# Optimization experiments

Hardware: AMD Instinct MI355X
Metric: run time of the kernel (lower is better)

Reference implementation:

```python
import jax, jax.numpy as jnp
import numpy as np

D_MODEL = 1024
N_HEADS = 8
D_HEAD = 64
D_FF = 4096
LAMBDA_INIT = 0.8
EPS = 1e-5


def _ln(x, g, b):
    m = jnp.mean(x, axis=-1, keepdims=True)
    v = jnp.mean(jnp.square(x - m), axis=-1, keepdims=True)
    return (x - m) * jax.lax.rsqrt(v + EPS) * g + b


def setup_inputs() -> dict:
    key = jax.random.key(0)
    ks = jax.random.split(key, 24)
    D, H, Dh, F = D_MODEL, N_HEADS, D_HEAD, D_FF
    P = 2 * H * Dh  # projection width for q/k/v (== D here)
    s = lambda fan: 1.0 / np.sqrt(fan)
    inp = {
        'x': jax.random.normal(ks[0], (2, 2048, D), jnp.float32),
        'ln1_g': jnp.ones((D,), jnp.float32), 'ln1_b': jnp.zeros((D,), jnp.float32),
        'ln2_g': jnp.ones((D,), jnp.float32), 'ln2_b': jnp.zeros((D,), jnp.float32),
        'Wq': jax.random.normal(ks[1], (D, P), jnp.float32) * s(D), 'bq': jnp.zeros((P,), jnp.float32),
        'Wk': jax.random.normal(ks[2], (D, P), jnp.float32) * s(D), 'bk': jnp.zeros((P,), jnp.float32),
        'Wv': jax.random.normal(ks[3], (D, P), jnp.float32) * s(D), 'bv': jnp.zeros((P,), jnp.float32),
        'Wo': jax.random.normal(ks[4], (P, D), jnp.float32) * s(P), 'bo': jnp.zeros((D,), jnp.float32),
        'lq1': jax.random.normal(ks[5], (H, Dh), jnp.float32) * 0.1,
        'lk1': jax.random.normal(ks[6], (H, Dh), jnp.float32) * 0.1,
        'lq2': jax.random.normal(ks[7], (H, Dh), jnp.float32) * 0.1,
        'lk2': jax.random.normal(ks[8], (H, Dh), jnp.float32) * 0.1,
        'gn_w': jnp.ones((P,), jnp.float32), 'gn_b': jnp.zeros((P,), jnp.float32),
        'W1': jax.random.normal(ks[9], (D, F), jnp.float32) * s(D), 'b1': jnp.zeros((F,), jnp.float32),
        'Wg': jax.random.normal(ks[10], (F, F), jnp.float32) * s(F), 'bg': jnp.zeros((F,), jnp.float32),
        'W2': jax.random.normal(ks[11], (F, D), jnp.float32) * s(F), 'b2': jnp.zeros((D,), jnp.float32),
    }
    return inp


def reference(x, ln1_g, ln1_b, ln2_g, ln2_b, Wq, bq, Wk, bk, Wv, bv, Wo, bo,
              lq1, lk1, lq2, lk2, gn_w, gn_b, W1, b1, Wg, bg, W2, b2):
    B, S, D = x.shape
    H, Dh = N_HEADS, D_HEAD
    scale = 1.0 / np.sqrt(Dh)

    # --- differential attention sublayer (pre-norm) ---
    h = _ln(x, ln1_g, ln1_b)
    q = (h @ Wq + bq).reshape(B, S, H, 2, Dh)
    k = (h @ Wk + bk).reshape(B, S, H, 2, Dh)
    v = (h @ Wv + bv).reshape(B, S, H, 2 * Dh)

    A1 = jax.nn.softmax(jnp.einsum('bshd,bthd->bhst', q[..., 0, :], k[..., 0, :]) * scale, axis=-1)
    A2 = jax.nn.softmax(jnp.einsum('bshd,bthd->bhst', q[..., 1, :], k[..., 1, :]) * scale, axis=-1)

    lam = (jnp.exp(jnp.sum(lq1 * lk1, axis=-1))
           - jnp.exp(jnp.sum(lq2 * lk2, axis=-1)) + LAMBDA_INIT)  # [H]
    diff = A1 - lam[None, :, None, None] * A2                     # [B,H,S,S]
    o = jnp.einsum('bhst,bthe->bshe', diff, v)                    # [B,S,H,2*Dh]

    # headwise GroupNorm over the 2*Dh channels of each head
    mu = jnp.mean(o, axis=-1, keepdims=True)
    var = jnp.mean(jnp.square(o - mu), axis=-1, keepdims=True)
    o = (o - mu) * jax.lax.rsqrt(var + EPS)
    o = o * gn_w.reshape(H, 2 * Dh) + gn_b.reshape(H, 2 * Dh)
    o = o * (1.0 - LAMBDA_INIT)

    attn_out = o.reshape(B, S, 2 * H * Dh) @ Wo + bo
    x = x + attn_out

    # --- FFN sublayer: note source applies prenorm2 BEFORE residual split ---
    x = _ln(x, ln2_g, ln2_b)
    u = x @ W1 + b1
    u = u * jax.nn.silu(u @ Wg + bg)   # swiGLU gate
    return x + (u @ W2 + b2)
```

## Files before the change

### kernel.cpp

```cpp
#include <hip/hip_runtime.h>
#include <hip/hip_bf16.h>


typedef __attribute__((ext_vector_type(8))) __bf16 bf16x8;
typedef __attribute__((ext_vector_type(4))) float f32x4;

#define GAS __attribute__((address_space(1)))
#define LAS __attribute__((address_space(3)))

__device__ __forceinline__ unsigned short f2bf(float f) {
  unsigned u = __float_as_uint(f);
  u += 0x7fffu + ((u >> 16) & 1u);
  return (unsigned short)(u >> 16);
}
__device__ __forceinline__ float bf2f(unsigned short s) {
  return __uint_as_float(((unsigned)s) << 16);
}

__global__ __launch_bounds__(256)
void transpose_cvt(const float* __restrict__ W, unsigned short* __restrict__ WT,
                   int K, int N, float scale) {
  __shared__ float tile[64][65];
  const int n0 = blockIdx.x * 64, k0 = blockIdx.y * 64;
  const int tr = threadIdx.x >> 4, tc = (threadIdx.x & 15) * 4;
#pragma unroll
  for (int i = 0; i < 4; ++i) {
    const float4 v = *(const float4*)&W[(size_t)(k0 + tr + i * 16) * N + n0 + tc];
    tile[tr + i * 16][tc + 0] = v.x;
    tile[tr + i * 16][tc + 1] = v.y;
    tile[tr + i * 16][tc + 2] = v.z;
    tile[tr + i * 16][tc + 3] = v.w;
  }
  __syncthreads();
#pragma unroll
  for (int i = 0; i < 4; ++i) {
    const int n = tr + i * 16;
    ushort4 o;
    o.x = f2bf(tile[tc + 0][n] * scale);
    o.y = f2bf(tile[tc + 1][n] * scale);
    o.z = f2bf(tile[tc + 2][n] * scale);
    o.w = f2bf(tile[tc + 3][n] * scale);
    *(ushort4*)&WT[(size_t)(n0 + n) * K + k0 + tc] = o;
  }
}

__global__ void prep_bias(const float* __restrict__ bq, const float* __restrict__ bk,
                          const float* __restrict__ bv, float* __restrict__ out,
                          float qscale) {
  const int i = blockIdx.x * 256 + threadIdx.x;
  if (i < 1024) out[i] = bq[i] * qscale;
  else if (i < 2048) out[i] = bk[i - 1024];
  else out[i] = bv[i - 2048];
}

__global__ __launch_bounds__(256)
void v_transpose(const unsigned short* __restrict__ v, unsigned short* __restrict__ VT) {
  __shared__ unsigned short tile[64][65];
  const int s0 = blockIdx.x * 64, e0 = blockIdx.y * 64, bh = blockIdx.z;
  const int b = bh >> 3, h = bh & 7;
  const int tr = threadIdx.x >> 4, tc = (threadIdx.x & 15) * 4;
  const size_t inbase = (size_t)b * 2048 * 3072 + h * 128;
#pragma unroll
  for (int i = 0; i < 4; ++i) {
    const int r = tr + i * 16;
    const ushort4 val = *(const ushort4*)&v[inbase + (size_t)(s0 + r) * 3072 + e0 + tc];
    tile[r][tc + 0] = val.x;
    tile[r][tc + 1] = val.y;
    tile[r][tc + 2] = val.z;
    tile[r][tc + 3] = val.w;
  }
  __syncthreads();
#pragma unroll
  for (int i = 0; i < 4; ++i) {
    const int n = tr + i * 16;
    ushort4 oo;
    oo.x = tile[tc + 0][n];
    oo.y = tile[tc + 1][n];
    oo.z = tile[tc + 2][n];
    oo.w = tile[tc + 3][n];
    *(ushort4*)&VT[(size_t)(bh * 128 + e0 + n) * 2048 + s0 + tc] = oo;
  }
}

__global__ void lam_kernel(const float* __restrict__ lq1, const float* __restrict__ lk1,
                           const float* __restrict__ lq2, const float* __restrict__ lk2,
                           float* __restrict__ lam) {
  const int w = threadIdx.x >> 6, d = threadIdx.x & 63;
  float a = lq1[w * 64 + d] * lk1[w * 64 + d];
  float c = lq2[w * 64 + d] * lk2[w * 64 + d];
#pragma unroll
  for (int off = 32; off; off >>= 1) {
    a += __shfl_xor(a, off);
    c += __shfl_xor(c, off);
  }
  if (d == 0) lam[w] = __expf(a) - __expf(c) + 0.8f;
}

template <int WRITE_F32>
__global__ __launch_bounds__(256)
void ln_kernel(const float* __restrict__ x, const float* __restrict__ g,
               const float* __restrict__ bsh, unsigned short* __restrict__ obf,
               float* __restrict__ of32) {
  __shared__ float red[16];
  const int row = blockIdx.x, tid = threadIdx.x;
  const float4 v = *(const float4*)&x[(size_t)row * 1024 + tid * 4];
  float s = v.x + v.y + v.z + v.w;
  float q = v.x * v.x + v.y * v.y + v.z * v.z + v.w * v.w;
#pragma unroll
  for (int off = 32; off; off >>= 1) {
    s += __shfl_xor(s, off);
    q += __shfl_xor(q, off);
  }
  if ((tid & 63) == 0) {
    red[tid >> 6] = s;
    red[8 + (tid >> 6)] = q;
  }
  __syncthreads();
  s = red[0] + red[1] + red[2] + red[3];
  q = red[8] + red[9] + red[10] + red[11];
  const float mean = s * (1.f / 1024.f);
  const float var = q * (1.f / 1024.f) - mean * mean;
  const float rstd = rsqrtf(var + 1e-5f);
  const float4 gg = *(const float4*)&g[tid * 4];
  const float4 bb = *(const float4*)&bsh[tid * 4];
  float y0 = (v.x - mean) * rstd * gg.x + bb.x;
  float y1 = (v.y - mean) * rstd * gg.y + bb.y;
  float y2 = (v.z - mean) * rstd * gg.z + bb.z;
  float y3 = (v.w - mean) * rstd * gg.w + bb.w;
  const size_t base = (size_t)row * 1024 + tid * 4;
  ushort4 o;
  o.x = f2bf(y0); o.y = f2bf(y1); o.z = f2bf(y2); o.w = f2bf(y3);
  *(ushort4*)&obf[base] = o;
  if (WRITE_F32) {
    *(float4*)&of32[base] = make_float4(y0, y1, y2, y3);
  }
}

template <int EPI>
__global__ __launch_bounds__(256)
void gemm_bf16(const unsigned short* __restrict__ A,
               const unsigned short* __restrict__ BT,
               const float* __restrict__ bias,
               const float* __restrict__ res,
               const unsigned short* __restrict__ gate_u,
               void* __restrict__ Cout, int M, int N, int K, float bscale) {
  __shared__ unsigned short ldsA[2][128 * 32];
  __shared__ unsigned short ldsB[2][128 * 32];
  const int tid = threadIdx.x;
  const int wv = tid >> 6, ln = tid & 63, lg = ln >> 4, lc = ln & 15;
  const int wm = wv >> 1, wn = wv & 1;
  const int nwg = gridDim.x * gridDim.y;
  const int linear = blockIdx.y * gridDim.x + blockIdx.x;
  const int swz = (linear & 7) * (nwg >> 3) + (linear >> 3);
  const int m0 = (swz / gridDim.x) * 128, n0 = (swz % gridDim.x) * 128;
  const int rsub = ln >> 2, acol = (ln & 3) * 8;

  f32x4 acc[4][4];
#pragma unroll
  for (int i = 0; i < 4; ++i)
#pragma unroll
    for (int j = 0; j < 4; ++j) acc[i][j] = (f32x4)0.f;

  auto stage = [&](int buf, int k0) {
#pragma unroll
    for (int j = 0; j < 2; ++j) {
      const int rowblk = wv * 32 + j * 16;
      const unsigned short* ga = A + (size_t)(m0 + rowblk + rsub) * K + (k0 + acol);
      __builtin_amdgcn_global_load_lds((GAS void*)ga,
          (LAS void*)&ldsA[buf][rowblk * 32], 16, 0, 0);
      const unsigned short* gb = BT + (size_t)(n0 + rowblk + rsub) * K + (k0 + acol);
      __builtin_amdgcn_global_load_lds((GAS void*)gb,
          (LAS void*)&ldsB[buf][rowblk * 32], 16, 0, 0);
    }
  };

  const int nk = K / 32;
  stage(0, 0);
  int cur = 0;
  for (int i = 0; i < nk; ++i) {
    if (i + 1 < nk) {
      stage(cur ^ 1, (i + 1) * 32);
      asm volatile("s_waitcnt vmcnt(4)" ::: "memory");
    } else {
      asm volatile("s_waitcnt vmcnt(0)" ::: "memory");
    }
    __builtin_amdgcn_s_barrier();
    bf16x8 af[4], bf[4];
#pragma unroll
    for (int m = 0; m < 4; ++m)
      af[m] = *(const bf16x8*)&ldsA[cur][(wm * 64 + m * 16 + lc) * 32 + lg * 8];
#pragma unroll
    for (int n = 0; n < 4; ++n)
      bf[n] = *(const bf16x8*)&ldsB[cur][(wn * 64 + n * 16 + lc) * 32 + lg * 8];
    __builtin_amdgcn_s_setprio(1);
#pragma unroll
    for (int m = 0; m < 4; ++m)
#pragma unroll
      for (int n = 0; n < 4; ++n)
        acc[m][n] = __builtin_amdgcn_mfma_f32_16x16x32_bf16(af[m], bf[n], acc[m][n], 0, 0, 0);
    __builtin_amdgcn_s_setprio(0);
    __builtin_amdgcn_s_barrier();
    cur ^= 1;
  }

#pragma unroll
  for (int m = 0; m < 4; ++m) {
#pragma unroll
    for (int n = 0; n < 4; ++n) {
      const int c = n0 + wn * 64 + n * 16 + lc;
      const float bc = bias[c] * bscale;
#pragma unroll
      for (int j = 0; j < 4; ++j) {
        const int r = m0 + wm * 64 + m * 16 + lg * 4 + j;
        const size_t idx = (size_t)r * N + c;
        const float v = acc[m][n][j] + bc;
        if (EPI == 0) {
          ((unsigned short*)Cout)[idx] = f2bf(v);
        } else if (EPI == 1) {
          ((float*)Cout)[idx] = res[idx] + v;
        } else {
          const float uu = bf2f(gate_u[idx]);
          const float sw = v / (1.f + __expf(-v));
          ((unsigned short*)Cout)[idx] = f2bf(uu * sw);
        }
      }
    }
  }
}

template <int EPI>
__global__ __launch_bounds__(512)
void gemm256(const unsigned short* __restrict__ A,
             const unsigned short* __restrict__ BT,
             const float* __restrict__ bias,
             const unsigned short* __restrict__ gate_u,
             unsigned short* __restrict__ Cout, int M, int N, int K) {
  __shared__ unsigned short lds[65536];
  const int tid = threadIdx.x;
  const int w = tid >> 6, ln = tid & 63, lg = ln >> 4, lc = ln & 15;
  const int wm = w >> 2, wn = w & 3;
  const int nwg = gridDim.x * gridDim.y;
  const int linear = blockIdx.y * gridDim.x + blockIdx.x;
  const int swzb = (linear & 7) * (nwg >> 3) + (linear >> 3);
  const int m0 = (swzb / gridDim.x) * 256, n0 = (swzb % gridDim.x) * 256;

  f32x4 acc[8][4];
#pragma unroll
  for (int i = 0; i < 8; ++i)
#pragma unroll
    for (int j = 0; j < 4; ++j) acc[i][j] = (f32x4)0.f;

  auto stage_half = [&](int tensor, int j, int hh) {
    const unsigned short* base = tensor ? BT : A;
    const int row0 = (tensor ? n0 : m0) + hh * 128;
    const int slot = tensor * 4 + (j & 1) * 2 + hh;
#pragma unroll
    for (int c = 0; c < 2; ++c) {
      const int chunk = w * 2 + c;
      const int L = chunk * 1024 + ln * 16;
      const int r = L >> 7, inner = L & 127;
      const char* src = (const char*)(base + (size_t)(row0 + r) * K + j * 64) +
                        (inner ^ ((r & 7) << 4));
      __builtin_amdgcn_global_load_lds((GAS void*)src,
          (LAS void*)((char*)lds + slot * 16384 + chunk * 1024), 16, 0, 0);
    }
  };
  auto read_a = [&](int j, int mf, int ks) -> bf16x8 {
    const int r = mf * 16 + lc;
    const int slot = (j & 1) * 2 + wm;
    const int cb = ks * 64 + lg * 16;
    return *(const bf16x8*)((const char*)lds + slot * 16384 + r * 128 +
                            (cb ^ ((r & 7) << 4)));
  };
  auto read_b = [&](int j, int nf, int ks) -> bf16x8 {
    const int R = wn * 64 + nf * 16 + lc;
    const int slot = 4 + (j & 1) * 2 + (R >> 7);
    const int r = R & 127;
    const int cb = ks * 64 + lg * 16;
    return *(const bf16x8*)((const char*)lds + slot * 16384 + r * 128 +
                            (cb ^ ((r & 7) << 4)));
  };

  const int nkt = K / 64;

  stage_half(0, 0, 0); stage_half(0, 0, 1);
  stage_half(1, 0, 0); stage_half(1, 0, 1);
  stage_half(1, 1, 0); stage_half(1, 1, 1);
  asm volatile("s_waitcnt vmcnt(0)" ::: "memory");
  __builtin_amdgcn_s_barrier();

  bf16x8 bfr[4][2];
  for (int it = 0; it < nkt / 2; ++it) {
    const int J = it * 2;
#pragma unroll
    for (int half = 0; half < 2; ++half) {
      const int jc = J + half;
#pragma unroll
      for (int q = 0; q < 4; ++q) {
        if (q == 0) {
#pragma unroll
          for (int nf = 0; nf < 4; ++nf)
#pragma unroll
            for (int ks = 0; ks < 2; ++ks) bfr[nf][ks] = read_b(jc, nf, ks);
        }
        bf16x8 afr[2][2];
#pragma unroll
        for (int mm = 0; mm < 2; ++mm)
#pragma unroll
          for (int ks = 0; ks < 2; ++ks) afr[mm][ks] = read_a(jc, q * 2 + mm, ks);
        if (half == 0) {
          if (q == 0) stage_half(0, J + 1, 0);
          if (q == 1) stage_half(0, J + 1, 1);
          if (q == 2 && J + 2 < nkt) stage_half(1, J + 2, 0);
          if (q == 3 && J + 2 < nkt) stage_half(1, J + 2, 1);
        } else {
          if (q == 0 && J + 2 < nkt) stage_half(0, J + 2, 0);
          if (q == 1 && J + 2 < nkt) stage_half(0, J + 2, 1);
          if (q == 2 && J + 3 < nkt) stage_half(1, J + 3, 0);
          if (q == 3 && J + 3 < nkt) stage_half(1, J + 3, 1);
        }
        if (q == 0) asm volatile("s_waitcnt lgkmcnt(8)" ::: "memory");
        if (q == 3) asm volatile("s_waitcnt vmcnt(4)" ::: "memory");
        __builtin_amdgcn_s_barrier();
        __builtin_amdgcn_s_setprio(1);
#pragma unroll
        for (int mm = 0; mm < 2; ++mm)
#pragma unroll
          for (int nf = 0; nf < 4; ++nf)
#pragma unroll
            for (int ks = 0; ks < 2; ++ks)
              acc[q * 2 + mm][nf] = __builtin_amdgcn_mfma_f32_16x16x32_bf16(
                  afr[mm][ks], bfr[nf][ks], acc[q * 2 + mm][nf], 0, 0, 0);
        __builtin_amdgcn_s_setprio(0);
        __builtin_amdgcn_s_barrier();
      }
    }
  }

#pragma unroll
  for (int mf = 0; mf < 8; ++mf) {
#pragma unroll
    for (int nf = 0; nf < 4; ++nf) {
      const int c = n0 + wn * 64 + nf * 16 + lc;
      const float bc = bias[c];
#pragma unroll
      for (int jj = 0; jj < 4; ++jj) {
        const int r = m0 + wm * 128 + mf * 16 + lg * 4 + jj;
        const size_t idx = (size_t)r * N + c;
        const float v = acc[mf][nf][jj] + bc;
        if (EPI == 0) {
          Cout[idx] = f2bf(v);
        } else {
          const float uu = bf2f(gate_u[idx]);
          const float sw = v / (1.f + __expf(-v));
          Cout[idx] = f2bf(uu * sw);
        }
      }
    }
  }
}

__global__ __launch_bounds__(256)
void attn_kernel(const unsigned short* __restrict__ q,
                 const unsigned short* __restrict__ k,
                 const unsigned short* __restrict__ VT,
                 float* __restrict__ Opart,
                 float* __restrict__ lsumPart) {
  constexpr int S = 2048;
  constexpr int QS = 3072;
  __shared__ unsigned short k_tile[2][32 * 128];
  __shared__ unsigned short v_tile[2][128 * 32];
  __shared__ unsigned short p_lds[4][2][512];
  const int tid = threadIdx.x, w = tid >> 6, ln = tid & 63, lg = ln >> 4, lc = ln & 15;
  const int id = blockIdx.x;
  const int bh = (id & 7) + 8 * ((id >> 9) & 1);
  const int qt = (id >> 3) & 31;
  const int tcn = (id >> 8) & 1;
  const size_t chan = (size_t)(bh >> 3) * S * QS + (bh & 7) * 128;
  const size_t vtbase = (size_t)bh * 128 * S;
  const int qrow = qt * 64 + w * 16 + lc;

  bf16x8 qf[2][2];
#pragma unroll
  for (int p = 0; p < 2; ++p)
#pragma unroll
    for (int ks = 0; ks < 2; ++ks)
      qf[p][ks] = *(const bf16x8*)&q[chan + (size_t)qrow * QS + p * 64 + ks * 32 + lg * 8];

  f32x4 O[2][8];
#pragma unroll
  for (int p = 0; p < 2; ++p)
#pragma unroll
    for (int ef = 0; ef < 8; ++ef) O[p][ef] = (f32x4)0.f;
  float lsum[2][4];
#pragma unroll
  for (int p = 0; p < 2; ++p)
#pragma unroll
    for (int j = 0; j < 4; ++j) lsum[p][j] = 0.f;

  const int prd = ((lc * 64 + lg * 16) ^ ((lc & 7) << 4)) >> 1;

  auto stage = [&](int buf, int t0) {
#pragma unroll
    for (int c = 0; c < 2; ++c) {
      {
        const int L = (w * 2 + c) * 1024 + ln * 16;
        const int r = L >> 8, inner = L & 255;
        const char* src = (const char*)(k + chan + (size_t)(t0 + r) * QS) +
                          (inner ^ ((r & 7) << 4));
        __builtin_amdgcn_global_load_lds((GAS void*)src,
            (LAS void*)((char*)&k_tile[buf][0] + (w * 2 + c) * 1024), 16, 0, 0);
      }
      {
        const int L = (w * 2 + c) * 1024 + ln * 16;
        const int e = L >> 6, inner = L & 63;
        const char* src = (const char*)(VT + vtbase + (size_t)e * S + t0) +
                          (inner ^ ((e & 3) << 4));
        __builtin_amdgcn_global_load_lds((GAS void*)src,
            (LAS void*)((char*)&v_tile[buf][0] + (w * 2 + c) * 1024), 16, 0, 0);
      }
    }
  };

  auto compute = [&](int buf) {
    const char* kb = (const char*)&k_tile[buf][0];
    const char* vb = (const char*)&v_tile[buf][0];
    bf16x8 vf[8];
#pragma unroll
    for (int ef = 0; ef < 8; ++ef) {
      const int e = ef * 16 + lc;
      vf[ef] = *(const bf16x8*)(vb + e * 64 + ((lg * 16) ^ ((e & 3) << 4)));
    }
#pragma unroll
    for (int p = 0; p < 2; ++p) {
      bf16x8 kf[2][2];
#pragma unroll
      for (int tf = 0; tf < 2; ++tf) {
        const int r = tf * 16 + lc;
#pragma unroll
        for (int ks = 0; ks < 2; ++ks)
          kf[tf][ks] = *(const bf16x8*)(kb + r * 256 +
                          ((p * 128 + ks * 64 + lg * 16) ^ ((r & 7) << 4)));
      }
      f32x4 sfr[2];
      __builtin_amdgcn_s_setprio(1);
#pragma unroll
      for (int tf = 0; tf < 2; ++tf) {
        f32x4 acc = (f32x4)0.f;
#pragma unroll
        for (int ks = 0; ks < 2; ++ks)
          acc = __builtin_amdgcn_mfma_f32_16x16x32_bf16(qf[p][ks], kf[tf][ks], acc, 0, 0, 0);
        sfr[tf] = acc;
      }
      __builtin_amdgcn_s_setprio(0);

#pragma unroll
      for (int tf = 0; tf < 2; ++tf)
#pragma unroll
        for (int j = 0; j < 4; ++j) {
          const float e = __expf(sfr[tf][j]);
          lsum[p][j] += e;
          const int qq = lg * 4 + j;
          const int wi = ((qq * 64 + (tf * 16 + lc) * 2) ^ ((qq & 7) << 4)) >> 1;
          p_lds[w][p][wi] = f2bf(e);
        }

      const bf16x8 pa = *(const bf16x8*)&p_lds[w][p][prd];
      __builtin_amdgcn_s_setprio(1);
#pragma unroll
      for (int ef = 0; ef < 8; ++ef)
        O[p][ef] = __builtin_amdgcn_mfma_f32_16x16x32_bf16(pa, vf[ef], O[p][ef], 0, 0, 0);
      __builtin_amdgcn_s_setprio(0);
    }
  };

  const int tbeg = tcn * (S / 2);
  stage(0, tbeg);
  int cur = 0;
  for (int it = 0; it < 32; ++it) {
    if (it < 31) {
      stage(cur ^ 1, tbeg + (it + 1) * 32);
      asm volatile("s_waitcnt vmcnt(4)" ::: "memory");
    } else {
      asm volatile("s_waitcnt vmcnt(0)" ::: "memory");
    }
    __builtin_amdgcn_s_barrier();
    compute(cur);
    __builtin_amdgcn_s_barrier();
    cur ^= 1;
  }

  const size_t rowbase = ((size_t)tcn * 16 + bh) * S;
#pragma unroll
  for (int p = 0; p < 2; ++p)
#pragma unroll
    for (int j = 0; j < 4; ++j) {
      float s = lsum[p][j];
      s += __shfl_xor(s, 1);
      s += __shfl_xor(s, 2);
      s += __shfl_xor(s, 4);
      s += __shfl_xor(s, 8);
      const int row = qt * 64 + w * 16 + lg * 4 + j;
      if (lc == 0)
        lsumPart[(rowbase + row) * 2 + p] = s;
#pragma unroll
      for (int ef = 0; ef < 8; ++ef)
        Opart[(rowbase + row) * 256 + p * 128 + ef * 16 + lc] = O[p][ef][j];
    }
}

__global__ __launch_bounds__(256)
void attn_reduce(const float* __restrict__ Opart, const float* __restrict__ lsumPart,
                 const float* __restrict__ lam,
                 const float* __restrict__ gn_w, const float* __restrict__ gn_b,
                 unsigned short* __restrict__ o) {
  constexpr int S = 2048;
  const int gw = (blockIdx.x * 256 + threadIdx.x) >> 6;
  const int ln = threadIdx.x & 63;
  const int bh = gw >> 11, s = gw & 2047;
  const int b = bh >> 3, h = bh & 7;
  const size_t r0 = ((size_t)bh * S + s) * 256;
  const size_t r1 = (((size_t)16 + bh) * S + s) * 256;
  const int e = ln * 2;
  const float2 o1a = *(const float2*)&Opart[r0 + e];
  const float2 o1b = *(const float2*)&Opart[r1 + e];
  const float2 o2a = *(const float2*)&Opart[r0 + 128 + e];
  const float2 o2b = *(const float2*)&Opart[r1 + 128 + e];
  const size_t l0 = ((size_t)bh * S + s) * 2;
  const size_t l1 = (((size_t)16 + bh) * S + s) * 2;
  const float inv1 = 1.f / (lsumPart[l0] + lsumPart[l1]);
  const float inv2 = lam[h] / (lsumPart[l0 + 1] + lsumPart[l1 + 1]);
  float d0 = (o1a.x + o1b.x) * inv1 - (o2a.x + o2b.x) * inv2;
  float d1 = (o1a.y + o1b.y) * inv1 - (o2a.y + o2b.y) * inv2;
  float sum = d0 + d1, sq = d0 * d0 + d1 * d1;
#pragma unroll
  for (int off = 32; off; off >>= 1) {
    sum += __shfl_xor(sum, off);
    sq += __shfl_xor(sq, off);
  }
  const float mean = sum * (1.f / 128.f);
  const float var = sq * (1.f / 128.f) - mean * mean;
  const float rstd = rsqrtf(var + 1e-5f);
  const float v0 = ((d0 - mean) * rstd * gn_w[h * 128 + e] + gn_b[h * 128 + e]) * 0.2f;
  const float v1 = ((d1 - mean) * rstd * gn_w[h * 128 + e + 1] + gn_b[h * 128 + e + 1]) * 0.2f;
  ushort2 ov;
  ov.x = f2bf(v0);
  ov.y = f2bf(v1);
  *(ushort2*)&o[(size_t)b * S * 1024 + (size_t)s * 1024 + h * 128 + e] = ov;
}

extern "C" void kernel_launch(void* const* d_in, const int* in_sizes, int n_in,
                              void* d_out, int out_size, void* d_ws, size_t ws_size,
                              hipStream_t stream) {
  (void)in_sizes; (void)n_in; (void)out_size; (void)ws_size;
  const float* x    = (const float*)d_in[0];
  const float* ln1g = (const float*)d_in[1];
  const float* ln1b = (const float*)d_in[2];
  const float* ln2g = (const float*)d_in[3];
  const float* ln2b = (const float*)d_in[4];
  const float* Wq   = (const float*)d_in[5];
  const float* bq   = (const float*)d_in[6];
  const float* Wk   = (const float*)d_in[7];
  const float* bk   = (const float*)d_in[8];
  const float* Wv   = (const float*)d_in[9];
  const float* bv   = (const float*)d_in[10];
  const float* Wo   = (const float*)d_in[11];
  const float* bo   = (const float*)d_in[12];
  const float* lq1  = (const float*)d_in[13];
  const float* lk1  = (const float*)d_in[14];
  const float* lq2  = (const float*)d_in[15];
  const float* lk2  = (const float*)d_in[16];
  const float* gnw  = (const float*)d_in[17];
  const float* gnb  = (const float*)d_in[18];
  const float* W1   = (const float*)d_in[19];
  const float* b1   = (const float*)d_in[20];
  const float* Wg   = (const float*)d_in[21];
  const float* bg   = (const float*)d_in[22];
  const float* W2   = (const float*)d_in[23];
  const float* b2   = (const float*)d_in[24];

  const int B = 2, S = 2048, D = 1024, F = 4096;
  const int M = B * S;
  const float qscale = 0.125f;

  char* ws = (char*)d_ws;
  size_t off = 0;
  auto alloc = [&](size_t bytes) {
    char* p = ws + off;
    off += (bytes + 255) & ~(size_t)255;
    return p;
  };
  unsigned short* WqkvT = (unsigned short*)alloc((size_t)3 * D * D * 2);
  unsigned short* WoT = (unsigned short*)alloc((size_t)D * D * 2);
  unsigned short* W1T = (unsigned short*)alloc((size_t)F * D * 2);
  unsigned short* WgT = (unsigned short*)alloc((size_t)F * F * 2);
  unsigned short* W2T = (unsigned short*)alloc((size_t)D * F * 2);
  float*          lamw= (float*)alloc(256);
  float*          bqkv= (float*)alloc(3072 * 4);
  unsigned short* h_bf= (unsigned short*)alloc((size_t)M * D * 2);
  unsigned short* qkv = (unsigned short*)alloc((size_t)M * 3 * D * 2);
  unsigned short* o_bf= (unsigned short*)alloc((size_t)M * D * 2);
  float*          x1  = (float*)alloc((size_t)M * D * 4);
  float*          x2  = (float*)alloc((size_t)M * D * 4);
  unsigned short* x2b = (unsigned short*)alloc((size_t)M * D * 2);
  unsigned short* u_bf= (unsigned short*)alloc((size_t)M * F * 2);
  float*          lsumP = (float*)alloc((size_t)2 * 16 * S * 2 * 4);
  unsigned short* w_bf= h_bf;

  float* Opart = (float*)x1;
  unsigned short* VT = u_bf + (size_t)12 * 1024 * 1024;

  transpose_cvt<<<dim3(D / 64, D / 64), 256, 0, stream>>>(Wq, WqkvT, D, D, qscale);
  transpose_cvt<<<dim3(D / 64, D / 64), 256, 0, stream>>>(Wk, WqkvT + (size_t)D * D, D, D, 1.0f);
  transpose_cvt<<<dim3(D / 64, D / 64), 256, 0, stream>>>(Wv, WqkvT + (size_t)2 * D * D, D, D, 1.0f);
  transpose_cvt<<<dim3(D / 64, D / 64), 256, 0, stream>>>(Wo, WoT, D, D, 1.0f);
  transpose_cvt<<<dim3(F / 64, D / 64), 256, 0, stream>>>(W1, W1T, D, F, 1.0f);
  transpose_cvt<<<dim3(F / 64, F / 64), 256, 0, stream>>>(Wg, WgT, F, F, 1.0f);
  transpose_cvt<<<dim3(D / 64, F / 64), 256, 0, stream>>>(W2, W2T, F, D, 1.0f);
  prep_bias<<<12, 256, 0, stream>>>(bq, bk, bv, bqkv, qscale);
  lam_kernel<<<1, 512, 0, stream>>>(lq1, lk1, lq2, lk2, lamw);

  ln_kernel<0><<<M, 256, 0, stream>>>(x, ln1g, ln1b, h_bf, nullptr);
  gemm256<0><<<dim3(3 * D / 256, M / 256), 512, 0, stream>>>(h_bf, WqkvT, bqkv, nullptr, qkv, M, 3 * D, D);
  v_transpose<<<dim3(S / 64, 2, 16), 256, 0, stream>>>(qkv + 2048, VT);
  attn_kernel<<<dim3(1024), 256, 0, stream>>>(qkv, qkv + 1024, VT, Opart, lsumP);
  attn_reduce<<<dim3(8192), 256, 0, stream>>>(Opart, lsumP, lamw, gnw, gnb, o_bf);
  gemm_bf16<1><<<dim3(D / 128, M / 128), 256, 0, stream>>>(o_bf, WoT, bo, x, nullptr, x1, M, D, D, 1.0f);

  ln_kernel<1><<<M, 256, 0, stream>>>(x1, ln2g, ln2b, x2b, x2);
  gemm256<0><<<dim3(F / 256, M / 256), 512, 0, stream>>>(x2b, W1T, b1, nullptr, u_bf, M, F, D);
  gemm256<2><<<dim3(F / 256, M / 256), 512, 0, stream>>>(u_bf, WgT, bg, u_bf, w_bf, M, F, F);
  gemm_bf16<1><<<dim3(D / 128, M / 128), 256, 0, stream>>>(w_bf, W2T, b2, x2, nullptr, (float*)d_out, M, D, F, 1.0f);
}
```

Measured before the change: 478.3 us.

## Use 128x64 tiles with swizzled LDS for N=1024 GEMMs and pack K contiguously

The two N=1024 GEMMs (Wo and W2 projections) switch from 128x128 to 128x64 tiles, which doubles the workgroup count from 256 to 512 so the CUs are better occupied. The LDS layout gets an XOR swizzle to reduce bank conflicts. A new k_pack kernel copies K per batch-head into a contiguous [bh, S, 128] buffer so attention reads it with a 256-byte row stride instead of 6 KB. In exchange, the smaller tiles reuse less data per load, and the extra packing kernel adds a launch plus memory traffic.

```diff
diff --git a/kernel.cpp b/kernel.cpp
--- a/kernel.cpp
+++ b/kernel.cpp
@@ -51,6 +51,16 @@
   if (i < 1024) out[i] = bq[i] * qscale;
   else if (i < 2048) out[i] = bk[i - 1024];
   else out[i] = bv[i - 2048];
+}
+
+__global__ __launch_bounds__(256)
+void k_pack(const unsigned short* __restrict__ qkv, unsigned short* __restrict__ KP) {
+  const int bh = blockIdx.y, b = bh >> 3, h = bh & 7;
+  const int s0 = blockIdx.x * 16;
+  const int sl = threadIdx.x >> 4, e8 = (threadIdx.x & 15) * 8;
+  const size_t src = (size_t)b * 2048 * 3072 + (size_t)(s0 + sl) * 3072 + 1024 + h * 128 + e8;
+  const size_t dst = ((size_t)bh * 2048 + s0 + sl) * 128 + e8;
+  *(uint4*)&KP[dst] = *(const uint4*)&qkv[src];
 }
 
 __global__ __launch_bounds__(256)
@@ -138,28 +148,29 @@
 
 template <int EPI>
 __global__ __launch_bounds__(256)
-void gemm_bf16(const unsigned short* __restrict__ A,
-               const unsigned short* __restrict__ BT,
-               const float* __restrict__ bias,
-               const float* __restrict__ res,
-               const unsigned short* __restrict__ gate_u,
-               void* __restrict__ Cout, int M, int N, int K, float bscale) {
+void gemm_n64(const unsigned short* __restrict__ A,
+              const unsigned short* __restrict__ BT,
+              const float* __restrict__ bias,
+              const float* __restrict__ res,
+              void* __restrict__ Cout, int M, int N, int K, float bscale) {
   __shared__ unsigned short ldsA[2][128 * 32];
-  __shared__ unsigned short ldsB[2][128 * 32];
+  __shared__ unsigned short ldsB[2][64 * 32];
   const int tid = threadIdx.x;
   const int wv = tid >> 6, ln = tid & 63, lg = ln >> 4, lc = ln & 15;
   const int wm = wv >> 1, wn = wv & 1;
   const int nwg = gridDim.x * gridDim.y;
   const int linear = blockIdx.y * gridDim.x + blockIdx.x;
   const int swz = (linear & 7) * (nwg >> 3) + (linear >> 3);
-  const int m0 = (swz / gridDim.x) * 128, n0 = (swz % gridDim.x) * 128;
-  const int rsub = ln >> 2, acol = (ln & 3) * 8;
-
-  f32x4 acc[4][4];
+  const int m0 = (swz / gridDim.x) * 128, n0 = (swz % gridDim.x) * 64;
+  const int rsub = ln >> 2;
+  const int sw_inner = ((ln & 3) * 16) ^ ((rsub & 3) << 4);
+  const int acol = sw_inner >> 1;
+
+  f32x4 acc[4][2];
 #pragma unroll
   for (int i = 0; i < 4; ++i)
 #pragma unroll
-    for (int j = 0; j < 4; ++j) acc[i][j] = (f32x4)0.f;
+    for (int j = 0; j < 2; ++j) acc[i][j] = (f32x4)0.f;
 
   auto stage = [&](int buf, int k0) {
 #pragma unroll
@@ -168,10 +179,10 @@
       const unsigned short* ga = A + (size_t)(m0 + rowblk + rsub) * K + (k0 + acol);
       __builtin_amdgcn_global_load_lds((GAS void*)ga,
           (LAS void*)&ldsA[buf][rowblk * 32], 16, 0, 0);
-      const unsigned short* gb = BT + (size_t)(n0 + rowblk + rsub) * K + (k0 + acol);
-      __builtin_amdgcn_global_load_lds((GAS void*)gb,
-          (LAS void*)&ldsB[buf][rowblk * 32], 16, 0, 0);
-    }
+    }
+    const unsigned short* gb = BT + (size_t)(n0 + wv * 16 + rsub) * K + (k0 + acol);
+    __builtin_amdgcn_global_load_lds((GAS void*)gb,
+        (LAS void*)&ldsB[buf][wv * 16 * 32], 16, 0, 0);
   };
 
   const int nk = K / 32;
@@ -180,23 +191,29 @@
   for (int i = 0; i < nk; ++i) {
     if (i + 1 < nk) {
       stage(cur ^ 1, (i + 1) * 32);
-      asm volatile("s_waitcnt vmcnt(4)" ::: "memory");
+      asm volatile("s_waitcnt vmcnt(3)" ::: "memory");
     } else {
       asm volatile("s_waitcnt vmcnt(0)" ::: "memory");
     }
     __builtin_amdgcn_s_barrier();
-    bf16x8 af[4], bf[4];
+    bf16x8 af[4], bf[2];
+#pragma unroll
+    for (int m = 0; m < 4; ++m) {
+      const int r = wm * 64 + m * 16 + lc;
+      af[m] = *(const bf16x8*)((const char*)&ldsA[cur][0] + r * 64 +
+                               ((lg * 16) ^ ((r & 3) << 4)));
+    }
+#pragma unroll
+    for (int n = 0; n < 2; ++n) {
+      const int r = wn * 32 + n * 16 + lc;
+      bf[n] = *(const bf16x8*)((const char*)&ldsB[cur][0] + r * 64 +
+                               ((lg * 16) ^ ((r & 3) << 4)));
+    }
+    __builtin_amdgcn_s_setprio(1);
 #pragma unroll
     for (int m = 0; m < 4; ++m)
-      af[m] = *(const bf16x8*)&ldsA[cur][(wm * 64 + m * 16 + lc) * 32 + lg * 8];
-#pragma unroll
-    for (int n = 0; n < 4; ++n)
-      bf[n] = *(const bf16x8*)&ldsB[cur][(wn * 64 + n * 16 + lc) * 32 + lg * 8];
-    __builtin_amdgcn_s_setprio(1);
-#pragma unroll
-    for (int m = 0; m < 4; ++m)
-#pragma unroll
-      for (int n = 0; n < 4; ++n)
+#pragma unroll
+      for (int n = 0; n < 2; ++n)
         acc[m][n] = __builtin_amdgcn_mfma_f32_16x16x32_bf16(af[m], bf[n], acc[m][n], 0, 0, 0);
     __builtin_amdgcn_s_setprio(0);
     __builtin_amdgcn_s_barrier();
@@ -206,22 +223,18 @@
 #pragma unroll
   for (int m = 0; m < 4; ++m) {
 #pragma unroll
-    for (int n = 0; n < 4; ++n) {
-      const int c = n0 + wn * 64 + n * 16 + lc;
+    for (int n = 0; n < 2; ++n) {
+      const int c = n0 + wn * 32 + n * 16 + lc;
       const float bc = bias[c] * bscale;
 #pragma unroll
       for (int j = 0; j < 4; ++j) {
         const int r = m0 + wm * 64 + m * 16 + lg * 4 + j;
         const size_t idx = (size_t)r * N + c;
         const float v = acc[m][n][j] + bc;
-        if (EPI == 0) {
-          ((unsigned short*)Cout)[idx] = f2bf(v);
-        } else if (EPI == 1) {
+        if (EPI == 1) {
           ((float*)Cout)[idx] = res[idx] + v;
         } else {
-          const float uu = bf2f(gate_u[idx]);
-          const float sw = v / (1.f + __expf(-v));
-          ((unsigned short*)Cout)[idx] = f2bf(uu * sw);
+          ((unsigned short*)Cout)[idx] = f2bf(v);
         }
       }
     }
@@ -362,7 +375,7 @@
 
 __global__ __launch_bounds__(256)
 void attn_kernel(const unsigned short* __restrict__ q,
-                 const unsigned short* __restrict__ k,
+                 const unsigned short* __restrict__ KP,
                  const unsigned short* __restrict__ VT,
                  float* __restrict__ Opart,
                  float* __restrict__ lsumPart) {
@@ -377,6 +390,7 @@
   const int qt = (id >> 3) & 31;
   const int tcn = (id >> 8) & 1;
   const size_t chan = (size_t)(bh >> 3) * S * QS + (bh & 7) * 128;
+  const size_t kpbase = (size_t)bh * S * 128;
   const size_t vtbase = (size_t)bh * 128 * S;
   const int qrow = qt * 64 + w * 16 + lc;
 
@@ -406,7 +420,7 @@
       {
         const int L = (w * 2 + c) * 1024 + ln * 16;
         const int r = L >> 8, inner = L & 255;
-        const char* src = (const char*)(k + chan + (size_t)(t0 + r) * QS) +
+        const char* src = (const char*)(KP + kpbase + (size_t)(t0 + r) * 128) +
                           (inner ^ ((r & 7) << 4));
         __builtin_amdgcn_global_load_lds((GAS void*)src,
             (LAS void*)((char*)&k_tile[buf][0] + (w * 2 + c) * 1024), 16, 0, 0);
@@ -609,6 +623,7 @@
 
   float* Opart = (float*)x1;
   unsigned short* VT = u_bf + (size_t)12 * 1024 * 1024;
+  unsigned short* KP = o_bf;
 
   transpose_cvt<<<dim3(D / 64, D / 64), 256, 0, stream>>>(Wq, WqkvT, D, D, qscale);
   transpose_cvt<<<dim3(D / 64, D / 64), 256, 0, stream>>>(Wk, WqkvT + (size_t)D * D, D, D, 1.0f);
@@ -622,13 +637,14 @@
 
   ln_kernel<0><<<M, 256, 0, stream>>>(x, ln1g, ln1b, h_bf, nullptr);
   gemm256<0><<<dim3(3 * D / 256, M / 256), 512, 0, stream>>>(h_bf, WqkvT, bqkv, nullptr, qkv, M, 3 * D, D);
+  k_pack<<<dim3(S / 16, 16), 256, 0, stream>>>(qkv, KP);
   v_transpose<<<dim3(S / 64, 2, 16), 256, 0, stream>>>(qkv + 2048, VT);
-  attn_kernel<<<dim3(1024), 256, 0, stream>>>(qkv, qkv + 1024, VT, Opart, lsumP);
+  attn_kernel<<<dim3(1024), 256, 0, stream>>>(qkv, KP, VT, Opart, lsumP);
   attn_reduce<<<dim3(8192), 256, 0, stream>>>(Opart, lsumP, lamw, gnw, gnb, o_bf);
-  gemm_bf16<1><<<dim3(D / 128, M / 128), 256, 0, stream>>>(o_bf, WoT, bo, x, nullptr, x1, M, D, D, 1.0f);
+  gemm_n64<1><<<dim3(D / 64, M / 128), 256, 0, stream>>>(o_bf, WoT, bo, x, x1, M, D, D, 1.0f);
 
   ln_kernel<1><<<M, 256, 0, stream>>>(x1, ln2g, ln2b, x2b, x2);
   gemm256<0><<<dim3(F / 256, M / 256), 512, 0, stream>>>(x2b, W1T, b1, nullptr, u_bf, M, F, D);
   gemm256<2><<<dim3(F / 256, M / 256), 512, 0, stream>>>(u_bf, WgT, bg, u_bf, w_bf, M, F, F);
-  gemm_bf16<1><<<dim3(D / 128, M / 128), 256, 0, stream>>>(w_bf, W2T, b2, x2, nullptr, (float*)d_out, M, D, F, 1.0f);
-}
+  gemm_n64<1><<<dim3(D / 64, M / 128), 256, 0, stream>>>(w_bf, W2T, b2, x2, (float*)d_out, M, D, F, 1.0f);
+}
```

Measured after the change: 464.4 us. 1.03x faster.
